# Performance work log

Measured on AMD Instinct MI355X. Metric: run time of the kernel, lower is better.

## Reference

```python
import jax, jax.numpy as jnp
import numpy as np

B, S, T = 2, 1024, 1024          # batch, new tokens, cache length (prefill: S == T)
DIM, NH, NKV, HD = 2048, 16, 4, 128
FFN = 5632
EPS = 1e-5
STD = 0.02


def rms_norm(x, w, eps=EPS):
    return x * jax.lax.rsqrt(jnp.mean(x * x, axis=-1, keepdims=True) + eps) * w


def apply_rope(x, freqs_cis):
    # x: [B, S, H, HD]; freqs_cis: [S, HD//2, 2] (cos, sin) over consecutive pairs
    xr = x.reshape(*x.shape[:-1], HD // 2, 2)
    cos = freqs_cis[None, :, None, :, 0]
    sin = freqs_cis[None, :, None, :, 1]
    x0, x1 = xr[..., 0], xr[..., 1]
    rot = jnp.stack([x0 * cos - x1 * sin, x0 * sin + x1 * cos], axis=-1)
    return rot.reshape(x.shape)


def setup_inputs() -> dict:
    key = jax.random.key(0)
    ks = jax.random.split(key, 10)
    x = jax.random.normal(ks[0], (B, S, DIM), jnp.float32)
    # rotary tables
    inv_freq = 1.0 / (10000.0 ** (np.arange(0, HD, 2, dtype=np.float32) / HD))
    ang = np.outer(np.arange(S, dtype=np.float32), inv_freq)          # [S, HD//2]
    freqs_cis = jnp.asarray(np.stack([np.cos(ang), np.sin(ang)], -1), jnp.float32)
    cache_k = jnp.zeros((1, B, T, NKV, HD), jnp.float32)
    cache_v = jnp.zeros((1, B, T, NKV, HD), jnp.float32)
    mask = jnp.triu(jnp.full((S, T), -1e9, jnp.float32), k=1)         # additive causal
    wq = jax.random.normal(ks[1], (DIM, NH, HD), jnp.float32) * STD
    wk = jax.random.normal(ks[2], (DIM, NKV, HD), jnp.float32) * STD
    wv = jax.random.normal(ks[3], (DIM, NKV, HD), jnp.float32) * STD
    wo = jax.random.normal(ks[4], (NH * HD, DIM), jnp.float32) * STD
    w_gate = jax.random.normal(ks[5], (DIM, FFN), jnp.float32) * STD
    w_up = jax.random.normal(ks[6], (DIM, FFN), jnp.float32) * STD
    w_down = jax.random.normal(ks[7], (FFN, DIM), jnp.float32) * STD
    attn_norm_w = jnp.ones((DIM,), jnp.float32)
    ffn_norm_w = jnp.ones((DIM,), jnp.float32)
    return dict(x=x, freqs_cis=freqs_cis, cache_k=cache_k, cache_v=cache_v,
                mask=mask, wq=wq, wk=wk, wv=wv, wo=wo, w_gate=w_gate,
                w_up=w_up, w_down=w_down, attn_norm_w=attn_norm_w,
                ffn_norm_w=ffn_norm_w, layer_idx=0)


def reference(x, freqs_cis, cache_k, cache_v, mask, wq, wk, wv, wo,
              w_gate, w_up, w_down, attn_norm_w, ffn_norm_w, layer_idx):
    # --- attention sub-block ---
    h = rms_norm(x, attn_norm_w)
    q = jnp.einsum('bsd,dhk->bshk', h, wq)          # [B,S,NH,HD]
    k = jnp.einsum('bsd,dgk->bsgk', h, wk)          # [B,S,NKV,HD]
    v = jnp.einsum('bsd,dgk->bsgk', h, wv)
    q = apply_rope(q, freqs_cis)
    k = apply_rope(k, freqs_cis)
    # append to per-layer KV cache at position 0 (prefill)
    cache_k = jax.lax.dynamic_update_slice(cache_k, k[None], (layer_idx, 0, 0, 0, 0))
    cache_v = jax.lax.dynamic_update_slice(cache_v, v[None], (layer_idx, 0, 0, 0, 0))
    keys = cache_k[layer_idx]                        # [B,T,NKV,HD]
    vals = cache_v[layer_idx]
    J = NH // NKV                                    # query heads per kv head
    qg = q.reshape(B, S, NKV, J, HD)
    scale = 1.0 / jnp.sqrt(jnp.float32(HD))
    scores = jnp.einsum('bsgjd,btgd->bgjst', qg, keys) * scale  # [B,NKV,J,S,T]
    scores = scores + mask                           # broadcast [S,T]
    probs = jax.nn.softmax(scores, axis=-1)
    ctx = jnp.einsum('bgjst,btgd->bsgjd', probs, vals).reshape(B, S, NH * HD)
    x = x + ctx @ wo
    # --- SwiGLU FFN sub-block ---
    hf = rms_norm(x, ffn_norm_w)
    ffn = (jax.nn.silu(hf @ w_gate) * (hf @ w_up)) @ w_down
    x = x + ffn
    return (x, cache_k, cache_v)
```

## Files before the change

kernel.cpp:

```cpp
#include <hip/hip_runtime.h>

typedef float f32x4 __attribute__((ext_vector_type(4)));
typedef __bf16 bf16x8 __attribute__((ext_vector_type(8)));
typedef unsigned short u16;

#define DIM 2048
#define SEQ 1024
#define BSZ 2
#define NH 16
#define NKV 4
#define HD 128
#define FFNDIM 5632
#define MROWS (BSZ * SEQ)

__device__ __forceinline__ u16 f2bf(float f) {
  union { float f; unsigned u; } v; v.f = f;
  unsigned u = v.u;
  unsigned r = (u + 0x7fffu + ((u >> 16) & 1u)) >> 16;
  return (u16)r;
}
__device__ __forceinline__ float bf2f(u16 h) {
  union { unsigned u; float f; } v; v.u = ((unsigned)h) << 16; return v.f;
}

__device__ __forceinline__ void gld16(const void* g, void* l) {
  __builtin_amdgcn_global_load_lds(
      (const __attribute__((address_space(1))) unsigned int*)g,
      (__attribute__((address_space(3))) unsigned int*)l, 16, 0, 0);
}

__global__ __launch_bounds__(256) void kxpose(const float* __restrict__ W,
                                              u16* __restrict__ Wt,
                                              int K, int N, int rs, int ro) {
  __shared__ float t[64][65];
  int kb = blockIdx.y * 64, nb = blockIdx.x * 64;
  int tid = threadIdx.x;
#pragma unroll
  for (int it = 0; it < 16; ++it) {
    int idx = it * 256 + tid;
    int r = idx >> 6, c = idx & 63;
    t[r][c] = W[(size_t)(kb + r) * N + nb + c];
  }
  __syncthreads();
#pragma unroll
  for (int it = 0; it < 16; ++it) {
    int idx = it * 256 + tid;
    int rn = idx >> 6, ck = idx & 63;
    Wt[((size_t)(nb + rn) * rs + ro) * K + kb + ck] = f2bf(t[ck][rn]);
  }
}

__global__ __launch_bounds__(256) void kvxpose(const u16* __restrict__ v,
                                               u16* __restrict__ vt) {
  __shared__ u16 t[64][66];
  int bg = blockIdx.z;
  int b = bg >> 2, g = bg & 3;
  int s0 = blockIdx.x * 64, d0 = blockIdx.y * 64;
  int tid = threadIdx.x;
  int rr = tid >> 4, cc = (tid & 15) * 4;
#pragma unroll
  for (int it = 0; it < 4; ++it) {
    int r = it * 16 + rr;
    *(uint2*)&t[r][cc] =
        *(const uint2*)(v + (size_t)(b * SEQ + s0 + r) * (NKV * HD) + g * HD + d0 + cc);
  }
  __syncthreads();
#pragma unroll
  for (int it = 0; it < 4; ++it) {
    int r = it * 16 + rr;
    u16 o[4] = {t[cc][r], t[cc + 1][r], t[cc + 2][r], t[cc + 3][r]};
    *(uint2*)(vt + (size_t)((b * NKV + g) * HD + d0 + r) * SEQ + s0 + cc) = *(const uint2*)o;
  }
}

__global__ __launch_bounds__(256) void krmsnorm(const float* __restrict__ x,
                                                const float* __restrict__ w,
                                                u16* __restrict__ out) {
  int row = blockIdx.x, tid = threadIdx.x;
  const float* xr = x + (size_t)row * DIM;
  float4 a = *(const float4*)(xr + tid * 8);
  float4 b = *(const float4*)(xr + tid * 8 + 4);
  float ss = a.x * a.x + a.y * a.y + a.z * a.z + a.w * a.w +
             b.x * b.x + b.y * b.y + b.z * b.z + b.w * b.w;
#pragma unroll
  for (int off = 1; off < 64; off <<= 1) ss += __shfl_xor(ss, off, 64);
  __shared__ float red[4];
  if ((tid & 63) == 0) red[tid >> 6] = ss;
  __syncthreads();
  float tot = red[0] + red[1] + red[2] + red[3];
  float sc = rsqrtf(tot * (1.0f / DIM) + 1e-5f);
  float xs[8] = {a.x, a.y, a.z, a.w, b.x, b.y, b.z, b.w};
  const float* wr = w + tid * 8;
  u16 o[8];
#pragma unroll
  for (int j = 0; j < 8; ++j) o[j] = f2bf(xs[j] * sc * wr[j]);
  *(int4*)(out + (size_t)row * DIM + tid * 8) = *(const int4*)o;
}

__global__ __launch_bounds__(256) void krope_q(u16* __restrict__ q,
                                               const float* __restrict__ fc) {
  int t = blockIdx.x * 256 + threadIdx.x;
  int j = t & 63;
  int h = (t >> 6) & (NH - 1);
  int row = t >> 10;
  int s = row & (SEQ - 1);
  size_t off = (size_t)row * DIM + h * HD + 2 * j;
  unsigned pk = *(unsigned*)(q + off);
  float x0 = bf2f((u16)pk), x1 = bf2f((u16)(pk >> 16));
  float cs = fc[s * HD + 2 * j], sn = fc[s * HD + 2 * j + 1];
  float y0 = x0 * cs - x1 * sn;
  float y1 = x0 * sn + x1 * cs;
  *(unsigned*)(q + off) = (unsigned)f2bf(y0) | ((unsigned)f2bf(y1) << 16);
}

__global__ __launch_bounds__(256) void krope_k(u16* __restrict__ k,
                                               const float* __restrict__ fc,
                                               float* __restrict__ ck) {
  int t = blockIdx.x * 256 + threadIdx.x;
  int j = t & 63;
  int g = (t >> 6) & (NKV - 1);
  int row = t >> 8;
  int s = row & (SEQ - 1);
  size_t off = (size_t)row * (NKV * HD) + g * HD + 2 * j;
  unsigned pk = *(unsigned*)(k + off);
  float x0 = bf2f((u16)pk), x1 = bf2f((u16)(pk >> 16));
  float cs = fc[s * HD + 2 * j], sn = fc[s * HD + 2 * j + 1];
  float y0 = x0 * cs - x1 * sn;
  float y1 = x0 * sn + x1 * cs;
  *(unsigned*)(k + off) = (unsigned)f2bf(y0) | ((unsigned)f2bf(y1) << 16);
  ck[off] = y0;
  ck[off + 1] = y1;
}

template <int EPI>
__global__ __launch_bounds__(512, 4) void kgemm(
    const u16* __restrict__ A, const u16* __restrict__ Bt, int N, int K,
    u16* o0, u16* __restrict__ o1, u16* __restrict__ o2,
    float* of, const float* res) {
  __shared__ u16 As[2][128 * 64];
  __shared__ u16 Bs[2][128 * 64];
  int bn = blockIdx.x * 128, bm = blockIdx.y * 128;
  int tid = threadIdx.x, lane = tid & 63, wv = tid >> 6;
  int wm = (wv >> 2) * 64;
  int wn = (wv & 3) * 32;
  int r16 = lane & 15, grp = lane >> 4;
  int srow = lane >> 3;
  int schunk = ((lane & 7) ^ srow) * 8;
  f32x4 acc[4][2] = {};
  const u16* Abase = A + (size_t)(bm + wv * 16) * K + schunk;
  const u16* Bbase = Bt + (size_t)(bn + wv * 16) * K + schunk;
  int woff = wv * 16 * 64;

  auto STAGE = [&](int buf, int k0) {
#pragma unroll
    for (int j = 0; j < 2; ++j) {
      gld16(Abase + (size_t)(j * 8 + srow) * K + k0, &As[buf][woff + j * 512]);
      gld16(Bbase + (size_t)(j * 8 + srow) * K + k0, &Bs[buf][woff + j * 512]);
    }
  };
  auto COMPUTE = [&](int buf) {
#pragma unroll
    for (int kk = 0; kk < 2; ++kk) {
      int swz = (((kk << 2) | grp) ^ (r16 & 7)) * 8;
      bf16x8 af[4], bfr[2];
#pragma unroll
      for (int m = 0; m < 4; ++m)
        af[m] = *(const bf16x8*)&As[buf][(wm + m * 16 + r16) * 64 + swz];
#pragma unroll
      for (int n = 0; n < 2; ++n)
        bfr[n] = *(const bf16x8*)&Bs[buf][(wn + n * 16 + r16) * 64 + swz];
#pragma unroll
      for (int m = 0; m < 4; ++m)
#pragma unroll
        for (int n = 0; n < 2; ++n)
          acc[m][n] = __builtin_amdgcn_mfma_f32_16x16x32_bf16(af[m], bfr[n], acc[m][n], 0, 0, 0);
    }
  };

  STAGE(0, 0);
  int nt = K >> 6;
  for (int t = 0; t < nt; ++t) {
    int cur = t & 1;
    if (t + 1 < nt) {
      STAGE(cur ^ 1, (t + 1) << 6);
      asm volatile("s_waitcnt vmcnt(4)" ::: "memory");
    } else {
      asm volatile("s_waitcnt vmcnt(0)" ::: "memory");
    }
    __builtin_amdgcn_sched_barrier(0);
    __builtin_amdgcn_s_barrier();
    __builtin_amdgcn_sched_barrier(0);
    COMPUTE(cur);
    __builtin_amdgcn_s_barrier();
  }

#pragma unroll
  for (int mi = 0; mi < 4; ++mi) {
#pragma unroll
    for (int ni = 0; ni < 2; ++ni) {
#pragma unroll
      for (int r = 0; r < 4; ++r) {
        int gr = bm + wm + mi * 16 + grp * 4 + r;
        int gc = bn + wn + ni * 16 + r16;
        float v = acc[mi][ni][r];
        if constexpr (EPI == 0) {
          if (gc < DIM) {
            o0[(size_t)gr * DIM + gc] = f2bf(v);
          } else if (gc < DIM + 512) {
            o1[(size_t)gr * 512 + (gc - DIM)] = f2bf(v);
          } else {
            int c2 = gc - (DIM + 512);
            of[(size_t)gr * 512 + c2] = v;
            o2[(size_t)gr * 512 + c2] = f2bf(v);
          }
        } else {
          of[(size_t)gr * N + gc] = v + res[(size_t)gr * N + gc];
        }
      }
    }
  }
}

__global__ __launch_bounds__(512, 4) void kgemm_gu(
    const u16* __restrict__ A, const u16* __restrict__ Bt,
    u16* __restrict__ out) {
  const int K = DIM;
  __shared__ u16 As[2][128 * 64];
  __shared__ u16 Bs[2][128 * 64];
  int bn = blockIdx.x * 128, bm = blockIdx.y * 128;
  int tid = threadIdx.x, lane = tid & 63, wv = tid >> 6;
  int wm = (wv >> 2) * 64;
  int wn = (wv & 3) * 32;
  int r16 = lane & 15, grp = lane >> 4;
  int srow = lane >> 3;
  int schunk = ((lane & 7) ^ srow) * 8;
  f32x4 acc[4][2] = {};
  const u16* Abase = A + (size_t)(bm + wv * 16) * K + schunk;
  const u16* Bbase = Bt + (size_t)(bn + wv * 16) * K + schunk;
  int woff = wv * 16 * 64;

  auto STAGE = [&](int buf, int k0) {
#pragma unroll
    for (int j = 0; j < 2; ++j) {
      gld16(Abase + (size_t)(j * 8 + srow) * K + k0, &As[buf][woff + j * 512]);
      gld16(Bbase + (size_t)(j * 8 + srow) * K + k0, &Bs[buf][woff + j * 512]);
    }
  };
  auto COMPUTE = [&](int buf) {
#pragma unroll
    for (int kk = 0; kk < 2; ++kk) {
      int swz = (((kk << 2) | grp) ^ (r16 & 7)) * 8;
      bf16x8 af[4], bfr[2];
#pragma unroll
      for (int m = 0; m < 4; ++m)
        af[m] = *(const bf16x8*)&As[buf][(wm + m * 16 + r16) * 64 + swz];
#pragma unroll
      for (int n = 0; n < 2; ++n)
        bfr[n] = *(const bf16x8*)&Bs[buf][(wn + n * 16 + r16) * 64 + swz];
#pragma unroll
      for (int m = 0; m < 4; ++m)
#pragma unroll
        for (int n = 0; n < 2; ++n)
          acc[m][n] = __builtin_amdgcn_mfma_f32_16x16x32_bf16(af[m], bfr[n], acc[m][n], 0, 0, 0);
    }
  };

  STAGE(0, 0);
  int nt = K >> 6;
  for (int t = 0; t < nt; ++t) {
    int cur = t & 1;
    if (t + 1 < nt) {
      STAGE(cur ^ 1, (t + 1) << 6);
      asm volatile("s_waitcnt vmcnt(4)" ::: "memory");
    } else {
      asm volatile("s_waitcnt vmcnt(0)" ::: "memory");
    }
    __builtin_amdgcn_sched_barrier(0);
    __builtin_amdgcn_s_barrier();
    __builtin_amdgcn_sched_barrier(0);
    COMPUTE(cur);
    __builtin_amdgcn_s_barrier();
  }

  bool evenlane = (r16 & 1) == 0;
#pragma unroll
  for (int mi = 0; mi < 4; ++mi) {
#pragma unroll
    for (int ni = 0; ni < 2; ++ni) {
#pragma unroll
      for (int r = 0; r < 4; ++r) {
        float v = acc[mi][ni][r];
        float pv = __shfl_xor(v, 1, 64);
        if (evenlane) {
          int gr = bm + wm + mi * 16 + grp * 4 + r;
          int gc = bn + wn + ni * 16 + r16;
          float sg = v / (1.0f + __expf(-v));
          out[(size_t)gr * FFNDIM + (gc >> 1)] = f2bf(sg * pv);
        }
      }
    }
  }
}

__global__ __launch_bounds__(64) void kattn(const u16* __restrict__ qb,
                                            const u16* __restrict__ kb,
                                            const u16* __restrict__ vtb,
                                            u16* __restrict__ ctxb) {
  __shared__ u16 Plds[16][40];
  int l = threadIdx.x;
  int qt = blockIdx.x, h = blockIdx.y, b = blockIdx.z;
  int g = h >> 2;
  int q0 = qt * 16;
  int r16 = l & 15, grp = l >> 4;
  const float scale = 0.08838834764831845f;
  bf16x8 qf[4];
  {
    const u16* qrow = qb + (size_t)(b * SEQ + q0 + r16) * DIM + h * HD + grp * 8;
#pragma unroll
    for (int c = 0; c < 4; ++c) qf[c] = *(const bf16x8*)(qrow + c * 32);
  }
  const u16* vt = vtb + (size_t)(b * NKV + g) * HD * SEQ;
  f32x4 ctx[8] = {};
  float m = -1e30f, lsum = 0.0f;
  int q_idx = q0 + r16;
  int ttmax = (q0 + 15) >> 5;
  for (int tt = 0; tt <= ttmax; ++tt) {
    int t0 = tt * 32;
    f32x4 d0 = {0.f, 0.f, 0.f, 0.f}, d1 = {0.f, 0.f, 0.f, 0.f};
    const u16* krow0 = kb + (size_t)(b * SEQ + t0 + r16) * (NKV * HD) + g * HD + grp * 8;
    const u16* krow1 = krow0 + 16 * (NKV * HD);
#pragma unroll
    for (int c = 0; c < 4; ++c) {
      bf16x8 kf0 = *(const bf16x8*)(krow0 + c * 32);
      d0 = __builtin_amdgcn_mfma_f32_16x16x32_bf16(kf0, qf[c], d0, 0, 0, 0);
      bf16x8 kf1 = *(const bf16x8*)(krow1 + c * 32);
      d1 = __builtin_amdgcn_mfma_f32_16x16x32_bf16(kf1, qf[c], d1, 0, 0, 0);
    }
    float p[8];
    float mx = -1e30f;
#pragma unroll
    for (int r = 0; r < 4; ++r) {
      int tA = t0 + grp * 4 + r;
      float sA = d0[r] * scale;
      if (tA > q_idx) sA = -1e30f;
      float sB = d1[r] * scale;
      if (tA + 16 > q_idx) sB = -1e30f;
      p[r] = sA; p[r + 4] = sB;
      mx = fmaxf(mx, fmaxf(sA, sB));
    }
    mx = fmaxf(mx, __shfl_xor(mx, 16, 64));
    mx = fmaxf(mx, __shfl_xor(mx, 32, 64));
    float mnew = fmaxf(m, mx);
    float psum = 0.f;
#pragma unroll
    for (int i = 0; i < 8; ++i) { p[i] = __expf(p[i] - mnew); psum += p[i]; }
    psum += __shfl_xor(psum, 16, 64);
    psum += __shfl_xor(psum, 32, 64);
    float corr = __expf(m - mnew);
    lsum = lsum * corr + psum;
    m = mnew;
    *(unsigned*)&Plds[r16][grp * 4] = (unsigned)f2bf(p[0]) | ((unsigned)f2bf(p[1]) << 16);
    *(unsigned*)&Plds[r16][grp * 4 + 2] = (unsigned)f2bf(p[2]) | ((unsigned)f2bf(p[3]) << 16);
    *(unsigned*)&Plds[r16][16 + grp * 4] = (unsigned)f2bf(p[4]) | ((unsigned)f2bf(p[5]) << 16);
    *(unsigned*)&Plds[r16][16 + grp * 4 + 2] = (unsigned)f2bf(p[6]) | ((unsigned)f2bf(p[7]) << 16);
    float cf[4];
#pragma unroll
    for (int r = 0; r < 4; ++r) cf[r] = __shfl(corr, grp * 4 + r, 64);
#pragma unroll
    for (int dc = 0; dc < 8; ++dc)
#pragma unroll
      for (int r = 0; r < 4; ++r) ctx[dc][r] *= cf[r];
    bf16x8 pa;
    {
      union { bf16x8 v; int4 q; } u;
      u.q = *(const int4*)&Plds[r16][grp * 8];
      pa = u.v;
    }
#pragma unroll
    for (int dc = 0; dc < 8; ++dc) {
      bf16x8 vf = *(const bf16x8*)(vt + (size_t)(dc * 16 + r16) * SEQ + t0 + grp * 8);
      ctx[dc] = __builtin_amdgcn_mfma_f32_16x16x32_bf16(pa, vf, ctx[dc], 0, 0, 0);
    }
  }
  float linv = 1.0f / lsum;
  float lf[4];
#pragma unroll
  for (int r = 0; r < 4; ++r) lf[r] = __shfl(linv, grp * 4 + r, 64);
  u16* crow = ctxb + (size_t)(b * SEQ + q0) * DIM + h * HD;
#pragma unroll
  for (int dc = 0; dc < 8; ++dc)
#pragma unroll
    for (int r = 0; r < 4; ++r)
      crow[(size_t)(grp * 4 + r) * DIM + dc * 16 + r16] = f2bf(ctx[dc][r] * lf[r]);
}

extern "C" void kernel_launch(void* const* d_in, const int* in_sizes, int n_in,
                              void* d_out, int out_size, void* d_ws, size_t ws_size,
                              hipStream_t stream) {
  const float* x = (const float*)d_in[0];
  const float* fc = (const float*)d_in[1];
  const float* wq = (const float*)d_in[5];
  const float* wk = (const float*)d_in[6];
  const float* wv = (const float*)d_in[7];
  const float* wo = (const float*)d_in[8];
  const float* wg = (const float*)d_in[9];
  const float* wu = (const float*)d_in[10];
  const float* wd = (const float*)d_in[11];
  const float* anw = (const float*)d_in[12];
  const float* fnw = (const float*)d_in[13];

  float* out_x = (float*)d_out;
  float* out_ck = out_x + (size_t)MROWS * DIM;
  float* out_cv = out_ck + (size_t)MROWS * NKV * HD;

  char* ws = (char*)d_ws;
  u16* h_b    = (u16*)(ws);
  u16* q_b    = (u16*)(ws + (8u << 20));
  u16* k_b    = (u16*)(ws + (16u << 20));
  u16* v_b    = (u16*)(ws + (18u << 20));
  u16* ctx_b  = (u16*)(ws + (20u << 20));
  u16* hf_b   = (u16*)(ws + (28u << 20));
  u16* Wt     = (u16*)(ws + (60u << 20));
  u16* vt_b   = h_b;
  u16* Wt_gu  = (u16*)(ws + (36u << 20));
  u16* g_b    = (u16*)(ws);
  u16* Wt_dn  = (u16*)(ws + (36u << 20));

  kxpose<<<dim3(2048 / 64, 2048 / 64), 256, 0, stream>>>(wq, Wt, 2048, 2048, 1, 0);
  kxpose<<<dim3(512 / 64, 2048 / 64), 256, 0, stream>>>(wk, Wt + (size_t)2048 * 2048, 2048, 512, 1, 0);
  kxpose<<<dim3(512 / 64, 2048 / 64), 256, 0, stream>>>(wv, Wt + (size_t)2560 * 2048, 2048, 512, 1, 0);

  krmsnorm<<<MROWS, 256, 0, stream>>>(x, anw, h_b);
  kgemm<0><<<dim3(3072 / 128, 16), 512, 0, stream>>>(h_b, Wt, 3072, 2048,
                                                     q_b, k_b, v_b, out_cv, nullptr);
  krope_q<<<8192, 256, 0, stream>>>(q_b, fc);
  krope_k<<<2048, 256, 0, stream>>>(k_b, fc, out_ck);
  kvxpose<<<dim3(SEQ / 64, HD / 64, BSZ * NKV), 256, 0, stream>>>(v_b, vt_b);
  kattn<<<dim3(SEQ / 16, NH, BSZ), 64, 0, stream>>>(q_b, k_b, vt_b, ctx_b);

  kxpose<<<dim3(32, 32), 256, 0, stream>>>(wo, Wt, 2048, 2048, 1, 0);
  kgemm<2><<<dim3(16, 16), 512, 0, stream>>>(ctx_b, Wt, 2048, 2048,
                                             nullptr, nullptr, nullptr, out_x, x);
  krmsnorm<<<MROWS, 256, 0, stream>>>(out_x, fnw, hf_b);

  kxpose<<<dim3(5632 / 64, 2048 / 64), 256, 0, stream>>>(wg, Wt_gu, 2048, 5632, 2, 0);
  kxpose<<<dim3(5632 / 64, 2048 / 64), 256, 0, stream>>>(wu, Wt_gu, 2048, 5632, 2, 1);
  kgemm_gu<<<dim3(11264 / 128, 16), 512, 0, stream>>>(hf_b, Wt_gu, g_b);
  kxpose<<<dim3(2048 / 64, 5632 / 64), 256, 0, stream>>>(wd, Wt_dn, 5632, 2048, 1, 0);
  kgemm<2><<<dim3(16, 16), 512, 0, stream>>>(g_b, Wt_dn, 2048, 5632,
                                             nullptr, nullptr, nullptr, out_x, out_x);
}
```

Measured before the change: 457.8 us.

## Widen attention key tile to 64, reverse query-tile order, lazy rescale

The attention kernel now handles 64 keys per iteration instead of 32, which halves the loop trip count and issues twice as many independent MFMAs per step. Query tiles are launched in reverse order so the heaviest causal tiles start first, which should balance load across CUs. The online-softmax rescale is skipped unless the running max grows by more than 8, and s_setprio is raised around the MFMA blocks. These changes cut per-iteration overhead and tail imbalance, at the cost of more registers and extra masked work on diagonal tiles.

```diff
diff --git a/kernel.cpp b/kernel.cpp
--- a/kernel.cpp
+++ b/kernel.cpp
@@ -306,9 +306,10 @@
                                             const u16* __restrict__ kb,
                                             const u16* __restrict__ vtb,
                                             u16* __restrict__ ctxb) {
-  __shared__ u16 Plds[16][40];
+  __shared__ u16 Plds[16][72];
   int l = threadIdx.x;
-  int qt = blockIdx.x, h = blockIdx.y, b = blockIdx.z;
+  int qt = gridDim.x - 1 - blockIdx.x;
+  int h = blockIdx.y, b = blockIdx.z;
   int g = h >> 2;
   int q0 = qt * 16;
   int r16 = l & 15, grp = l >> 4;
@@ -323,64 +324,83 @@
   f32x4 ctx[8] = {};
   float m = -1e30f, lsum = 0.0f;
   int q_idx = q0 + r16;
-  int ttmax = (q0 + 15) >> 5;
+  int ttmax = (q0 + 15) >> 6;
   for (int tt = 0; tt <= ttmax; ++tt) {
-    int t0 = tt * 32;
-    f32x4 d0 = {0.f, 0.f, 0.f, 0.f}, d1 = {0.f, 0.f, 0.f, 0.f};
-    const u16* krow0 = kb + (size_t)(b * SEQ + t0 + r16) * (NKV * HD) + g * HD + grp * 8;
-    const u16* krow1 = krow0 + 16 * (NKV * HD);
+    int t0 = tt * 64;
+    f32x4 d[4] = {{0.f, 0.f, 0.f, 0.f}, {0.f, 0.f, 0.f, 0.f},
+                  {0.f, 0.f, 0.f, 0.f}, {0.f, 0.f, 0.f, 0.f}};
+    const u16* kbase = kb + (size_t)(b * SEQ + t0 + r16) * (NKV * HD) + g * HD + grp * 8;
+    __builtin_amdgcn_s_setprio(1);
 #pragma unroll
     for (int c = 0; c < 4; ++c) {
-      bf16x8 kf0 = *(const bf16x8*)(krow0 + c * 32);
-      d0 = __builtin_amdgcn_mfma_f32_16x16x32_bf16(kf0, qf[c], d0, 0, 0, 0);
-      bf16x8 kf1 = *(const bf16x8*)(krow1 + c * 32);
-      d1 = __builtin_amdgcn_mfma_f32_16x16x32_bf16(kf1, qf[c], d1, 0, 0, 0);
-    }
-    float p[8];
+#pragma unroll
+      for (int ch = 0; ch < 4; ++ch) {
+        bf16x8 kf = *(const bf16x8*)(kbase + (size_t)(ch * 16) * (NKV * HD) + c * 32);
+        d[ch] = __builtin_amdgcn_mfma_f32_16x16x32_bf16(kf, qf[c], d[ch], 0, 0, 0);
+      }
+    }
+    __builtin_amdgcn_s_setprio(0);
+    float p[16];
     float mx = -1e30f;
 #pragma unroll
-    for (int r = 0; r < 4; ++r) {
-      int tA = t0 + grp * 4 + r;
-      float sA = d0[r] * scale;
-      if (tA > q_idx) sA = -1e30f;
-      float sB = d1[r] * scale;
-      if (tA + 16 > q_idx) sB = -1e30f;
-      p[r] = sA; p[r + 4] = sB;
-      mx = fmaxf(mx, fmaxf(sA, sB));
+    for (int ch = 0; ch < 4; ++ch) {
+#pragma unroll
+      for (int r = 0; r < 4; ++r) {
+        int tA = t0 + ch * 16 + grp * 4 + r;
+        float s = d[ch][r] * scale;
+        if (tA > q_idx) s = -1e30f;
+        p[ch * 4 + r] = s;
+        mx = fmaxf(mx, s);
+      }
     }
     mx = fmaxf(mx, __shfl_xor(mx, 16, 64));
     mx = fmaxf(mx, __shfl_xor(mx, 32, 64));
-    float mnew = fmaxf(m, mx);
+    if (!__all(mx - m <= 8.0f)) {
+      float mnew = fmaxf(m, mx);
+      float corr = __expf(m - mnew);
+      lsum *= corr;
+      float cf[4];
+#pragma unroll
+      for (int r = 0; r < 4; ++r) cf[r] = __shfl(corr, grp * 4 + r, 64);
+#pragma unroll
+      for (int dc = 0; dc < 8; ++dc)
+#pragma unroll
+        for (int r = 0; r < 4; ++r) ctx[dc][r] *= cf[r];
+      m = mnew;
+    }
     float psum = 0.f;
 #pragma unroll
-    for (int i = 0; i < 8; ++i) { p[i] = __expf(p[i] - mnew); psum += p[i]; }
+    for (int i = 0; i < 16; ++i) {
+      p[i] = __expf(p[i] - m);
+      psum += p[i];
+    }
     psum += __shfl_xor(psum, 16, 64);
     psum += __shfl_xor(psum, 32, 64);
-    float corr = __expf(m - mnew);
-    lsum = lsum * corr + psum;
-    m = mnew;
-    *(unsigned*)&Plds[r16][grp * 4] = (unsigned)f2bf(p[0]) | ((unsigned)f2bf(p[1]) << 16);
-    *(unsigned*)&Plds[r16][grp * 4 + 2] = (unsigned)f2bf(p[2]) | ((unsigned)f2bf(p[3]) << 16);
-    *(unsigned*)&Plds[r16][16 + grp * 4] = (unsigned)f2bf(p[4]) | ((unsigned)f2bf(p[5]) << 16);
-    *(unsigned*)&Plds[r16][16 + grp * 4 + 2] = (unsigned)f2bf(p[6]) | ((unsigned)f2bf(p[7]) << 16);
-    float cf[4];
-#pragma unroll
-    for (int r = 0; r < 4; ++r) cf[r] = __shfl(corr, grp * 4 + r, 64);
-#pragma unroll
-    for (int dc = 0; dc < 8; ++dc)
-#pragma unroll
-      for (int r = 0; r < 4; ++r) ctx[dc][r] *= cf[r];
-    bf16x8 pa;
+    lsum += psum;
+#pragma unroll
+    for (int ch = 0; ch < 4; ++ch) {
+      unsigned w0 = (unsigned)f2bf(p[ch * 4]) | ((unsigned)f2bf(p[ch * 4 + 1]) << 16);
+      unsigned w1 = (unsigned)f2bf(p[ch * 4 + 2]) | ((unsigned)f2bf(p[ch * 4 + 3]) << 16);
+      *(unsigned*)&Plds[r16][ch * 16 + grp * 4] = w0;
+      *(unsigned*)&Plds[r16][ch * 16 + grp * 4 + 2] = w1;
+    }
+    bf16x8 pa0, pa1;
     {
-      union { bf16x8 v; int4 q; } u;
-      u.q = *(const int4*)&Plds[r16][grp * 8];
-      pa = u.v;
-    }
+      union { bf16x8 v; int4 q; } u0, u1;
+      u0.q = *(const int4*)&Plds[r16][grp * 8];
+      u1.q = *(const int4*)&Plds[r16][32 + grp * 8];
+      pa0 = u0.v;
+      pa1 = u1.v;
+    }
+    __builtin_amdgcn_s_setprio(1);
 #pragma unroll
     for (int dc = 0; dc < 8; ++dc) {
-      bf16x8 vf = *(const bf16x8*)(vt + (size_t)(dc * 16 + r16) * SEQ + t0 + grp * 8);
-      ctx[dc] = __builtin_amdgcn_mfma_f32_16x16x32_bf16(pa, vf, ctx[dc], 0, 0, 0);
-    }
+      bf16x8 vf0 = *(const bf16x8*)(vt + (size_t)(dc * 16 + r16) * SEQ + t0 + grp * 8);
+      bf16x8 vf1 = *(const bf16x8*)(vt + (size_t)(dc * 16 + r16) * SEQ + t0 + 32 + grp * 8);
+      ctx[dc] = __builtin_amdgcn_mfma_f32_16x16x32_bf16(pa0, vf0, ctx[dc], 0, 0, 0);
+      ctx[dc] = __builtin_amdgcn_mfma_f32_16x16x32_bf16(pa1, vf1, ctx[dc], 0, 0, 0);
+    }
+    __builtin_amdgcn_s_setprio(0);
   }
   float linv = 1.0f / lsum;
   float lf[4];
```

Result: no change. 462.9 us (+1.1%).
